# Kernel tuning notes

Hardware: AMD Instinct MI355X
Metric: run time of the kernel (lower is better)

Reference implementation:

```python
import jax, jax.numpy as jnp
import numpy as np

NUM_EXPERTS = 8
IN_FEATURES = 2048
OUT_FEATURES = 5632
GROUP_SIZE = 64
NUM_TOKENS = 4096


def setup_inputs() -> dict:
    key = jax.random.key(0)
    k1, k2, k3, k4 = jax.random.split(key, 4)
    inp = jax.random.normal(k1, (NUM_TOKENS, IN_FEATURES), dtype=jnp.float32)
    # tokens are pre-sorted contiguously per expert; balanced routing
    tokens_per_expert = jnp.full((NUM_EXPERTS,), NUM_TOKENS // NUM_EXPERTS, dtype=jnp.int32)
    # int4 quantized weights stored as integer codes in [0, 16)
    weights = jax.random.randint(k2, (NUM_EXPERTS, IN_FEATURES, OUT_FEATURES), 0, 16, dtype=jnp.int32)
    n_groups = IN_FEATURES // GROUP_SIZE
    scales = jax.random.uniform(k3, (NUM_EXPERTS, n_groups, OUT_FEATURES, 1), dtype=jnp.float32,
                                minval=0.005, maxval=0.02)
    zeros = jax.random.normal(k4, (NUM_EXPERTS, n_groups, OUT_FEATURES, 1), dtype=jnp.float32) * 0.01
    scales_and_zeros = jnp.concatenate([scales, zeros], axis=-1)  # [E, K//G, N, 2]
    return {"input": inp, "tokens_per_expert": tokens_per_expert,
            "weights": weights, "scales_and_zeros": scales_and_zeros}


def _dequant(weights, scales_and_zeros):
    # torchao int4 convention: w = (q - 8) * scale + zero, grouped along K
    E, K, N = weights.shape
    n_groups = scales_and_zeros.shape[1]
    g = K // n_groups
    q = weights.astype(jnp.float32).reshape(E, n_groups, g, N)
    s = scales_and_zeros[..., 0][:, :, None, :]  # [E, K//G, 1, N]
    z = scales_and_zeros[..., 1][:, :, None, :]
    return ((q - 8.0) * s + z).reshape(E, K, N)


def reference(input, tokens_per_expert, weights, scales_and_zeros):
    num_tokens, K = input.shape
    E = weights.shape[0]
    W = _dequant(weights, scales_and_zeros)  # [E, K, N] float32
    # expert id of each (contiguous-sorted) token from cumsum boundaries
    cum = jnp.cumsum(tokens_per_expert)                      # [E]
    seg = jnp.searchsorted(cum, jnp.arange(num_tokens), side='right')  # [T]
    start = jnp.concatenate([jnp.zeros((1,), cum.dtype), cum[:-1]])
    pos = jnp.arange(num_tokens) - start[seg]                # slot within expert block
    # capacity-based grouped GEMM (balanced routing in setup: C = T // E)
    C = num_tokens // E
    buf = jnp.zeros((E, C, K), input.dtype).at[seg, pos].set(input)
    y = jnp.einsum('eck,ekn->ecn', buf, W)                   # per-expert GEMM
    return y[seg, pos]                                       # [T, N]
```

## Files before the change

kernel.cpp:

```cpp
#include <hip/hip_runtime.h>

#define NE    8
#define KDIM  2048
#define NDIM  5632
#define NTOK  4096
#define CAP   512
#define NGRP  32
#define BM    128
#define BN    128
#define BK    32
#define MT    4
#define NT    44
#define LDSS  40

#define K8      (KDIM / 8)
#define NBLK_N  (NDIM / 256)
#define PACK_BLOCKS (NE * K8 * NBLK_N)
#define ACV_BLOCKS  (NTOK * KDIM / (8 * 256))
#define PACKED_BYTES ((size_t)NE * K8 * NDIM * 4)
#define ABF_BYTES    ((size_t)NTOK * KDIM * 2)
#define WBT_BYTES    ((size_t)NE * NDIM * KDIM * 2)

#define KT_DQ (KDIM / 128)
#define NT_DQ (NDIM / 128)
#define DQT_BLOCKS (NE * KT_DQ * NT_DQ)

typedef __attribute__((ext_vector_type(8))) short bf16x8;
typedef __attribute__((ext_vector_type(4))) short bf16x4;
typedef __attribute__((ext_vector_type(4))) float f32x4;

static __device__ __forceinline__ short f2bf(float f) {
    union { float f; unsigned u; } x; x.f = f;
    unsigned r = (x.u + 0x7fffu + ((x.u >> 16) & 1u)) >> 16;
    return (short)r;
}

static __device__ __forceinline__ void gl2lds16(const unsigned short* g, short* l) {
    __builtin_amdgcn_global_load_lds(
        (const __attribute__((address_space(1))) unsigned int*)g,
        (__attribute__((address_space(3))) unsigned int*)l, 16, 0, 0);
}

__global__ __launch_bounds__(256)
void dq_kernel(const int* __restrict__ wq, const float* __restrict__ sz,
               const float* __restrict__ inp,
               unsigned short* __restrict__ wbt, unsigned short* __restrict__ abf)
{
    const int bid = blockIdx.x;
    if (bid < DQT_BLOCKS) {
        const int e  = bid / (KT_DQ * NT_DQ);
        const int r  = bid % (KT_DQ * NT_DQ);
        const int kt = r / NT_DQ;
        const int ntb = r % NT_DQ;
        const int k0 = kt * 128;
        const int n0 = ntb * 128;
        const int t  = threadIdx.x;

        __shared__ __align__(16) short T[128 * 128];

        const int col  = t & 31;
        const int band = t >> 5;
        const int g    = (k0 >> 6) + (band >> 2);

        float s_[4], z_[4];
        #pragma unroll
        for (int j = 0; j < 4; ++j) {
            const int n = n0 + col * 4 + j;
            const float2 s2 = *(const float2*)(sz + (((size_t)e * NGRP + g) * NDIM + n) * 2);
            s_[j] = s2.x;
            z_[j] = s2.y - 8.f * s2.x;
        }

        const int* src = wq + ((size_t)e * KDIM + k0 + band * 16) * NDIM + n0 + col * 4;

        #pragma unroll
        for (int p4 = 0; p4 < 4; ++p4) {
            int4 v0 = *(const int4*)(src + (size_t)(p4 * 4 + 0) * NDIM);
            int4 v1 = *(const int4*)(src + (size_t)(p4 * 4 + 1) * NDIM);
            int4 v2 = *(const int4*)(src + (size_t)(p4 * 4 + 2) * NDIM);
            int4 v3 = *(const int4*)(src + (size_t)(p4 * 4 + 3) * NDIM);
            const int kb = band * 16 + p4 * 4;
            const int slotbase = kb >> 3;
            const int halfoff  = (kb & 7);

            #pragma unroll
            for (int j = 0; j < 4; ++j) {
                const int q0 = (j == 0) ? v0.x : (j == 1) ? v0.y : (j == 2) ? v0.z : v0.w;
                const int q1 = (j == 0) ? v1.x : (j == 1) ? v1.y : (j == 2) ? v1.z : v1.w;
                const int q2 = (j == 0) ? v2.x : (j == 1) ? v2.y : (j == 2) ? v2.z : v2.w;
                const int q3 = (j == 0) ? v3.x : (j == 1) ? v3.y : (j == 2) ? v3.z : v3.w;
                bf16x4 quad;
                quad[0] = f2bf(fmaf((float)q0, s_[j], z_[j]));
                quad[1] = f2bf(fmaf((float)q1, s_[j], z_[j]));
                quad[2] = f2bf(fmaf((float)q2, s_[j], z_[j]));
                quad[3] = f2bf(fmaf((float)q3, s_[j], z_[j]));
                const int n_l = col * 4 + j;
                const int addr = n_l * 128 + ((slotbase ^ (n_l & 15)) << 3) + halfoff;
                *(bf16x4*)&T[addr] = quad;
            }
        }

        __syncthreads();

        const int wc = t & 7;
        const int wn = t >> 3;
        #pragma unroll
        for (int p = 0; p < 4; ++p) {
            const int n_l = wn + p * 32;
            const int x = n_l & 15;
            unsigned short* dst = wbt + ((size_t)e * NDIM + n0 + n_l) * KDIM + k0;
            const bf16x8 r0 = *(const bf16x8*)&T[n_l * 128 + ((wc ^ x) << 3)];
            const bf16x8 r1 = *(const bf16x8*)&T[n_l * 128 + (((wc + 8) ^ x) << 3)];
            *(bf16x8*)(dst + wc * 8) = r0;
            *(bf16x8*)(dst + (wc + 8) * 8) = r1;
        }
    } else {
        const size_t t = (size_t)(bid - DQT_BLOCKS) * 256 + threadIdx.x;
        const float4* p = (const float4*)inp + t * 2;
        const float4 v0 = p[0], v1 = p[1];
        bf16x8 h;
        h[0] = f2bf(v0.x); h[1] = f2bf(v0.y); h[2] = f2bf(v0.z); h[3] = f2bf(v0.w);
        h[4] = f2bf(v1.x); h[5] = f2bf(v1.y); h[6] = f2bf(v1.z); h[7] = f2bf(v1.w);
        *((bf16x8*)abf + t) = h;
    }
}

__global__ __launch_bounds__(256)
void hqq_gemm3(const unsigned short* __restrict__ abf,
               const unsigned short* __restrict__ wbt,
               float* __restrict__ out)
{
    const int bid = blockIdx.x;
    const int e   = bid & 7;
    const int rem = bid >> 3;
    const int nt  = rem >> 2;
    const int mt  = rem & 3;

    __shared__ __align__(16) short Alds[BM * BK];
    __shared__ __align__(16) short Blds[BN * BK];

    const int tid = threadIdx.x;
    const int m0  = e * CAP + mt * BM;
    const int n0  = nt * BN;

    const unsigned short* Ab = abf + (size_t)m0 * KDIM;
    const unsigned short* Bb = wbt + ((size_t)e * NDIM + n0) * KDIM;

    f32x4 acc[4][4];
    #pragma unroll
    for (int i = 0; i < 4; ++i)
        #pragma unroll
        for (int j = 0; j < 4; ++j)
            acc[i][j] = (f32x4){0.f, 0.f, 0.f, 0.f};

    const int wave = tid >> 6;
    const int lane = tid & 63;
    const int wm = (wave >> 1) << 6;
    const int wn = (wave & 1) << 6;
    const int lr = lane & 15;
    const int lq = lane >> 4;

    for (int k0 = 0; k0 < KDIM; k0 += BK) {
        #pragma unroll
        for (int p = 0; p < 2; ++p) {
            const int idx = p * 256 + tid;
            const int row = idx >> 2;
            const int kq  = idx & 3;
            gl2lds16(Ab + (size_t)row * KDIM + k0 + kq * 8, &Alds[idx * 8]);
            gl2lds16(Bb + (size_t)row * KDIM + k0 + kq * 8, &Blds[idx * 8]);
        }
        __syncthreads();

        bf16x8 af[4], bv[4];
        #pragma unroll
        for (int i = 0; i < 4; ++i)
            af[i] = *(const bf16x8*)&Alds[(wm + i * 16 + lr) * BK + lq * 8];
        #pragma unroll
        for (int j = 0; j < 4; ++j)
            bv[j] = *(const bf16x8*)&Blds[(wn + j * 16 + lr) * BK + lq * 8];
        #pragma unroll
        for (int i = 0; i < 4; ++i)
            #pragma unroll
            for (int j = 0; j < 4; ++j)
                acc[i][j] = __builtin_amdgcn_mfma_f32_16x16x32_bf16(af[i], bv[j], acc[i][j], 0, 0, 0);

        __syncthreads();
    }

    const int orow0 = m0 + wm + lq * 4;
    const int ocol0 = n0 + wn + lr;
    #pragma unroll
    for (int i = 0; i < 4; ++i)
        #pragma unroll
        for (int r = 0; r < 4; ++r) {
            float* op = out + (size_t)(orow0 + i * 16 + r) * NDIM + ocol0;
            #pragma unroll
            for (int j = 0; j < 4; ++j)
                op[j * 16] = acc[i][j][r];
        }
}

__global__ __launch_bounds__(256)
void pack_kernel(const int* __restrict__ wq, const float* __restrict__ inp,
                 unsigned* __restrict__ pw, unsigned short* __restrict__ abf)
{
    const int bid = blockIdx.x;
    if (bid < PACK_BLOCKS) {
        const int e  = bid / (K8 * NBLK_N);
        const int r  = bid % (K8 * NBLK_N);
        const int k8 = r / NBLK_N;
        const int nb = r % NBLK_N;
        const int n  = nb * 256 + threadIdx.x;
        const int* src = wq + ((size_t)e * KDIM + k8 * 8) * NDIM + n;
        unsigned v = 0;
        #pragma unroll
        for (int j = 0; j < 8; ++j)
            v |= (unsigned)(src[(size_t)j * NDIM] & 15) << (4 * j);
        pw[((size_t)e * K8 + k8) * NDIM + n] = v;
    } else {
        const size_t t = (size_t)(bid - PACK_BLOCKS) * 256 + threadIdx.x;
        const float4* p = (const float4*)inp + t * 2;
        const float4 v0 = p[0], v1 = p[1];
        bf16x8 h;
        h[0] = f2bf(v0.x); h[1] = f2bf(v0.y); h[2] = f2bf(v0.z); h[3] = f2bf(v0.w);
        h[4] = f2bf(v1.x); h[5] = f2bf(v1.y); h[6] = f2bf(v1.z); h[7] = f2bf(v1.w);
        *((bf16x8*)abf + t) = h;
    }
}

__global__ __launch_bounds__(256, 2)
void hqq_gemm2(const unsigned short* __restrict__ abf,
               const unsigned*       __restrict__ pw,
               const float*          __restrict__ sz,
               float*                __restrict__ out)
{
    const int bid = blockIdx.x;
    const int e   = bid / (MT * NT);
    const int rem = bid % (MT * NT);
    const int nt  = rem >> 2;
    const int mt  = rem & 3;

    __shared__ __align__(16) short Alds[BM * LDSS];
    __shared__ __align__(16) short Blds[BN * LDSS];

    const int tid = threadIdx.x;
    const int m0  = e * CAP + mt * BM;
    const int n0  = nt * BN;

    const int a_kq  = tid & 3;
    const int a_row = tid >> 2;
    const int b_n   = tid & 127;
    const int b_h   = tid >> 7;

    const unsigned short* Ab = abf + (size_t)m0 * KDIM;
    const unsigned*       Wb = pw  + (size_t)e * K8 * NDIM + n0 + b_n;
    const float*          SZb = sz + (size_t)e * NGRP * (NDIM * 2) + (size_t)(n0 + b_n) * 2;

    f32x4 acc[4][4];
    #pragma unroll
    for (int i = 0; i < 4; ++i)
        #pragma unroll
        for (int j = 0; j < 4; ++j)
            acc[i][j] = (f32x4){0.f, 0.f, 0.f, 0.f};

    const int wave = tid >> 6;
    const int lane = tid & 63;
    const int wm = (wave >> 1) << 6;
    const int wn = (wave & 1) << 6;
    const int lr = lane & 15;
    const int lq = lane >> 4;

    for (int k0 = 0; k0 < KDIM; k0 += BK) {
        const int g = k0 >> 6;
        #pragma unroll
        for (int p = 0; p < 2; ++p) {
            const int row = a_row + p * 64;
            const bf16x8 v = *(const bf16x8*)(Ab + (size_t)row * KDIM + k0 + a_kq * 8);
            *(bf16x8*)&Alds[row * LDSS + a_kq * 8] = v;
        }
        const float2 s2 = *(const float2*)(SZb + (size_t)g * (NDIM * 2));
        const float s  = s2.x;
        const float z8 = s2.y - 8.f * s2.x;
        const unsigned* wp = Wb + ((size_t)(k0 >> 3) + b_h * 2) * NDIM;
        const unsigned u0 = wp[0];
        const unsigned u1 = wp[NDIM];
        bf16x8 bb0, bb1;
        #pragma unroll
        for (int j = 0; j < 8; ++j) {
            bb0[j] = f2bf(fmaf((float)((u0 >> (4 * j)) & 15u), s, z8));
            bb1[j] = f2bf(fmaf((float)((u1 >> (4 * j)) & 15u), s, z8));
        }
        *(bf16x8*)&Blds[b_n * LDSS + b_h * 16]     = bb0;
        *(bf16x8*)&Blds[b_n * LDSS + b_h * 16 + 8] = bb1;

        __syncthreads();

        bf16x8 af[4], bfv[4];
        #pragma unroll
        for (int i = 0; i < 4; ++i)
            af[i] = *(const bf16x8*)&Alds[(wm + i * 16 + lr) * LDSS + lq * 8];
        #pragma unroll
        for (int j = 0; j < 4; ++j)
            bfv[j] = *(const bf16x8*)&Blds[(wn + j * 16 + lr) * LDSS + lq * 8];
        #pragma unroll
        for (int i = 0; i < 4; ++i)
            #pragma unroll
            for (int j = 0; j < 4; ++j)
                acc[i][j] = __builtin_amdgcn_mfma_f32_16x16x32_bf16(af[i], bfv[j], acc[i][j], 0, 0, 0);

        __syncthreads();
    }

    const int orow0 = m0 + wm + lq * 4;
    const int ocol0 = n0 + wn + lr;
    #pragma unroll
    for (int i = 0; i < 4; ++i)
        #pragma unroll
        for (int r = 0; r < 4; ++r) {
            float* op = out + (size_t)(orow0 + i * 16 + r) * NDIM + ocol0;
            #pragma unroll
            for (int j = 0; j < 4; ++j)
                op[j * 16] = acc[i][j][r];
        }
}

__global__ __launch_bounds__(256, 2)
void hqq_gemm_fallback(const float* __restrict__ inp,
                       const int*   __restrict__ wq,
                       const float* __restrict__ sz,
                       float*       __restrict__ out)
{
    const int bid = blockIdx.x;
    const int e   = bid / (MT * NT);
    const int rem = bid % (MT * NT);
    const int nt  = rem >> 2;
    const int mt  = rem & 3;

    __shared__ __align__(16) short Alds[BM * LDSS];
    __shared__ __align__(16) short Blds[BN * LDSS];

    const int tid = threadIdx.x;
    const int m0  = e * CAP + mt * BM;
    const int n0  = nt * BN;

    const int a_kq  = tid & 7;
    const int a_row = tid >> 3;
    const int b_n   = tid & 127;
    const int b_h   = tid >> 7;

    const float* Ab  = inp + (size_t)m0 * KDIM;
    const int*   Wb  = wq  + (size_t)e * KDIM * NDIM + n0 + b_n;
    const float* SZb = sz  + (size_t)e * NGRP * (NDIM * 2) + (size_t)(n0 + b_n) * 2;

    f32x4 acc[4][4];
    #pragma unroll
    for (int i = 0; i < 4; ++i)
        #pragma unroll
        for (int j = 0; j < 4; ++j)
            acc[i][j] = (f32x4){0.f, 0.f, 0.f, 0.f};

    const int wave = tid >> 6;
    const int lane = tid & 63;
    const int wm = (wave >> 1) << 6;
    const int wn = (wave & 1) << 6;
    const int lr = lane & 15;
    const int lq = lane >> 4;

    for (int k0 = 0; k0 < KDIM; k0 += BK) {
        const int g = k0 >> 6;
        #pragma unroll
        for (int p = 0; p < 4; ++p) {
            const int row = a_row + p * 32;
            const float4 v = *(const float4*)(Ab + (size_t)row * KDIM + k0 + a_kq * 4);
            bf16x4 h;
            h[0] = f2bf(v.x); h[1] = f2bf(v.y); h[2] = f2bf(v.z); h[3] = f2bf(v.w);
            *(bf16x4*)&Alds[row * LDSS + a_kq * 4] = h;
        }
        const float2 s2 = *(const float2*)(SZb + (size_t)g * (NDIM * 2));
        const float s  = s2.x;
        const float z8 = s2.y - 8.f * s2.x;
        #pragma unroll
        for (int oo = 0; oo < 2; ++oo) {
            const int ko = b_h * 8 + oo * 16;
            const int* wp = Wb + (size_t)(k0 + ko) * NDIM;
            bf16x8 bb;
            #pragma unroll
            for (int j = 0; j < 8; ++j) {
                const float q = (float)wp[(size_t)j * NDIM];
                bb[j] = f2bf(fmaf(q, s, z8));
            }
            *(bf16x8*)&Blds[b_n * LDSS + ko] = bb;
        }
        __syncthreads();
        bf16x8 af[4], bfv[4];
        #pragma unroll
        for (int i = 0; i < 4; ++i)
            af[i] = *(const bf16x8*)&Alds[(wm + i * 16 + lr) * LDSS + lq * 8];
        #pragma unroll
        for (int j = 0; j < 4; ++j)
            bfv[j] = *(const bf16x8*)&Blds[(wn + j * 16 + lr) * LDSS + lq * 8];
        #pragma unroll
        for (int i = 0; i < 4; ++i)
            #pragma unroll
            for (int j = 0; j < 4; ++j)
                acc[i][j] = __builtin_amdgcn_mfma_f32_16x16x32_bf16(af[i], bfv[j], acc[i][j], 0, 0, 0);
        __syncthreads();
    }

    const int orow0 = m0 + wm + lq * 4;
    const int ocol0 = n0 + wn + lr;
    #pragma unroll
    for (int i = 0; i < 4; ++i)
        #pragma unroll
        for (int r = 0; r < 4; ++r) {
            float* op = out + (size_t)(orow0 + i * 16 + r) * NDIM + ocol0;
            #pragma unroll
            for (int j = 0; j < 4; ++j)
                op[j * 16] = acc[i][j][r];
        }
}

extern "C" void kernel_launch(void* const* d_in, const int* in_sizes, int n_in,
                              void* d_out, int out_size, void* d_ws, size_t ws_size,
                              hipStream_t stream) {
    const float* inp = (const float*)d_in[0];
    const int*   wq  = (const int*)d_in[2];
    const float* sz  = (const float*)d_in[3];
    float*       out = (float*)d_out;

    if (ws_size >= ABF_BYTES + WBT_BYTES) {
        unsigned short* abf = (unsigned short*)d_ws;
        unsigned short* wbt = (unsigned short*)((char*)d_ws + ABF_BYTES);
        dq_kernel<<<dim3(DQT_BLOCKS + ACV_BLOCKS), dim3(256), 0, stream>>>(wq, sz, inp, wbt, abf);
        hqq_gemm3<<<dim3(NE * MT * NT), dim3(256), 0, stream>>>(abf, wbt, out);
    } else if (ws_size >= PACKED_BYTES + ABF_BYTES) {
        unsigned*       pw  = (unsigned*)d_ws;
        unsigned short* abf = (unsigned short*)((char*)d_ws + PACKED_BYTES);
        pack_kernel<<<dim3(PACK_BLOCKS + ACV_BLOCKS), dim3(256), 0, stream>>>(wq, inp, pw, abf);
        hqq_gemm2<<<dim3(NE * MT * NT), dim3(256), 0, stream>>>(abf, pw, sz, out);
    } else {
        hqq_gemm_fallback<<<dim3(NE * MT * NT), dim3(256), 0, stream>>>(inp, wq, sz, out);
    }
}
```

Baseline: 738.1 us.

## Double-buffer LDS tiles in grouped GEMM to overlap loads with MFMA

Turns the shared-memory A/B tiles into two ping-pong buffers and issues the next k-tile's global-to-LDS copies before the current tile is consumed by MFMAs. This removes one barrier per iteration and is meant to hide global-load latency behind compute. It also adds a launch-bounds occupancy hint of 3 blocks per CU. The cost is doubled LDS use, which may reduce occupancy, and correctness now depends on the async LDS writes being complete by the single remaining barrier.

```diff
diff --git a/kernel.cpp b/kernel.cpp
--- a/kernel.cpp
+++ b/kernel.cpp
@@ -125,7 +125,7 @@
     }
 }
 
-__global__ __launch_bounds__(256)
+__global__ __launch_bounds__(256, 3)
 void hqq_gemm3(const unsigned short* __restrict__ abf,
                const unsigned short* __restrict__ wbt,
                float* __restrict__ out)
@@ -136,8 +136,8 @@
     const int nt  = rem >> 2;
     const int mt  = rem & 3;
 
-    __shared__ __align__(16) short Alds[BM * BK];
-    __shared__ __align__(16) short Blds[BN * BK];
+    __shared__ __align__(16) short Alds[2][BM * BK];
+    __shared__ __align__(16) short Blds[2][BN * BK];
 
     const int tid = threadIdx.x;
     const int m0  = e * CAP + mt * BM;
@@ -160,24 +160,35 @@
     const int lr = lane & 15;
     const int lq = lane >> 4;
 
+    const int r0_ = tid >> 2;
+    const int kq_ = tid & 3;
+
+    {
+        gl2lds16(Ab + (size_t)r0_ * KDIM + kq_ * 8,        &Alds[0][tid * 8]);
+        gl2lds16(Bb + (size_t)r0_ * KDIM + kq_ * 8,        &Blds[0][tid * 8]);
+        gl2lds16(Ab + (size_t)(r0_ + 64) * KDIM + kq_ * 8, &Alds[0][(256 + tid) * 8]);
+        gl2lds16(Bb + (size_t)(r0_ + 64) * KDIM + kq_ * 8, &Blds[0][(256 + tid) * 8]);
+    }
+    __syncthreads();
+
+    int cur = 0;
     for (int k0 = 0; k0 < KDIM; k0 += BK) {
-        #pragma unroll
-        for (int p = 0; p < 2; ++p) {
-            const int idx = p * 256 + tid;
-            const int row = idx >> 2;
-            const int kq  = idx & 3;
-            gl2lds16(Ab + (size_t)row * KDIM + k0 + kq * 8, &Alds[idx * 8]);
-            gl2lds16(Bb + (size_t)row * KDIM + k0 + kq * 8, &Blds[idx * 8]);
-        }
-        __syncthreads();
+        if (k0 + BK < KDIM) {
+            const int kn = k0 + BK;
+            const int nb = cur ^ 1;
+            gl2lds16(Ab + (size_t)r0_ * KDIM + kn + kq_ * 8,        &Alds[nb][tid * 8]);
+            gl2lds16(Bb + (size_t)r0_ * KDIM + kn + kq_ * 8,        &Blds[nb][tid * 8]);
+            gl2lds16(Ab + (size_t)(r0_ + 64) * KDIM + kn + kq_ * 8, &Alds[nb][(256 + tid) * 8]);
+            gl2lds16(Bb + (size_t)(r0_ + 64) * KDIM + kn + kq_ * 8, &Blds[nb][(256 + tid) * 8]);
+        }
 
         bf16x8 af[4], bv[4];
         #pragma unroll
         for (int i = 0; i < 4; ++i)
-            af[i] = *(const bf16x8*)&Alds[(wm + i * 16 + lr) * BK + lq * 8];
-        #pragma unroll
-        for (int j = 0; j < 4; ++j)
-            bv[j] = *(const bf16x8*)&Blds[(wn + j * 16 + lr) * BK + lq * 8];
+            af[i] = *(const bf16x8*)&Alds[cur][(wm + i * 16 + lr) * BK + lq * 8];
+        #pragma unroll
+        for (int j = 0; j < 4; ++j)
+            bv[j] = *(const bf16x8*)&Blds[cur][(wn + j * 16 + lr) * BK + lq * 8];
         #pragma unroll
         for (int i = 0; i < 4; ++i)
             #pragma unroll
@@ -185,6 +196,7 @@
                 acc[i][j] = __builtin_amdgcn_mfma_f32_16x16x32_bf16(af[i], bv[j], acc[i][j], 0, 0, 0);
 
         __syncthreads();
+        cur ^= 1;
     }
 
     const int orow0 = m0 + wm + lq * 4;
```

Result: faster. 699.4 us (-5.3%).

## Triple-buffer LDS tiles in grouped GEMM with async prefetch two stages ahead

Applied to the files above, without the earlier changes.

Replaces the single-buffered LDS load/compute loop with a three-stage ring of A/B tiles. Global-to-LDS loads for tile k+2 are issued before the MFMAs on tile k, and partial vmcnt waits plus a single barrier per iteration replace the two syncthreads. The goal is to hide global memory latency behind matrix math. It triples LDS use (about 48KB per block) and adds an occupancy hint of 3 blocks per CU, which may constrain registers.

```diff
diff --git a/kernel.cpp b/kernel.cpp
--- a/kernel.cpp
+++ b/kernel.cpp
@@ -125,7 +125,7 @@
     }
 }
 
-__global__ __launch_bounds__(256)
+__global__ __launch_bounds__(256, 3)
 void hqq_gemm3(const unsigned short* __restrict__ abf,
                const unsigned short* __restrict__ wbt,
                float* __restrict__ out)
@@ -136,8 +136,8 @@
     const int nt  = rem >> 2;
     const int mt  = rem & 3;
 
-    __shared__ __align__(16) short Alds[BM * BK];
-    __shared__ __align__(16) short Blds[BN * BK];
+    __shared__ __align__(16) short Alds[3][BM * BK];
+    __shared__ __align__(16) short Blds[3][BN * BK];
 
     const int tid = threadIdx.x;
     const int m0  = e * CAP + mt * BM;
@@ -160,32 +160,53 @@
     const int lr = lane & 15;
     const int lq = lane >> 4;
 
+    const int r0_ = tid >> 2;
+    const int kq_ = tid & 3;
+
+#define STAGE3(kk, Adst, Bdst)                                                       \
+    do {                                                                             \
+        gl2lds16(Ab + (size_t)r0_ * KDIM + (kk) + kq_ * 8,        (Adst) + tid * 8); \
+        gl2lds16(Bb + (size_t)r0_ * KDIM + (kk) + kq_ * 8,        (Bdst) + tid * 8); \
+        gl2lds16(Ab + (size_t)(r0_ + 64) * KDIM + (kk) + kq_ * 8, (Adst) + (256 + tid) * 8); \
+        gl2lds16(Bb + (size_t)(r0_ + 64) * KDIM + (kk) + kq_ * 8, (Bdst) + (256 + tid) * 8); \
+    } while (0)
+
+    short* Ac = &Alds[0][0]; short* An = &Alds[1][0]; short* Af = &Alds[2][0];
+    short* Bc = &Blds[0][0]; short* Bn = &Blds[1][0]; short* Bf = &Blds[2][0];
+
+    STAGE3(0,  Ac, Bc);
+    STAGE3(BK, An, Bn);
+
     for (int k0 = 0; k0 < KDIM; k0 += BK) {
-        #pragma unroll
-        for (int p = 0; p < 2; ++p) {
-            const int idx = p * 256 + tid;
-            const int row = idx >> 2;
-            const int kq  = idx & 3;
-            gl2lds16(Ab + (size_t)row * KDIM + k0 + kq * 8, &Alds[idx * 8]);
-            gl2lds16(Bb + (size_t)row * KDIM + k0 + kq * 8, &Blds[idx * 8]);
-        }
-        __syncthreads();
+        if (k0 + BK < KDIM) {
+            asm volatile("s_waitcnt vmcnt(4)" ::: "memory");
+        } else {
+            asm volatile("s_waitcnt vmcnt(0)" ::: "memory");
+        }
+        __builtin_amdgcn_s_barrier();
+        asm volatile("" ::: "memory");
+        __builtin_amdgcn_sched_barrier(0);
+
+        if (k0 + 2 * BK < KDIM)
+            STAGE3(k0 + 2 * BK, Af, Bf);
 
         bf16x8 af[4], bv[4];
         #pragma unroll
         for (int i = 0; i < 4; ++i)
-            af[i] = *(const bf16x8*)&Alds[(wm + i * 16 + lr) * BK + lq * 8];
-        #pragma unroll
-        for (int j = 0; j < 4; ++j)
-            bv[j] = *(const bf16x8*)&Blds[(wn + j * 16 + lr) * BK + lq * 8];
+            af[i] = *(const bf16x8*)&Ac[(wm + i * 16 + lr) * BK + lq * 8];
+        #pragma unroll
+        for (int j = 0; j < 4; ++j)
+            bv[j] = *(const bf16x8*)&Bc[(wn + j * 16 + lr) * BK + lq * 8];
         #pragma unroll
         for (int i = 0; i < 4; ++i)
             #pragma unroll
             for (int j = 0; j < 4; ++j)
                 acc[i][j] = __builtin_amdgcn_mfma_f32_16x16x32_bf16(af[i], bv[j], acc[i][j], 0, 0, 0);
 
-        __syncthreads();
-    }
+        short* tA = Ac; Ac = An; An = Af; Af = tA;
+        short* tB = Bc; Bc = Bn; Bn = Bf; Bf = tB;
+    }
+#undef STAGE3
 
     const int orow0 = m0 + wm + lq * 4;
     const int ocol0 = n0 + wn + lr;
```

Result: faster. 692.6 us (-6.2%).
